# Kernel optimization log

Hardware: AMD Instinct MI355X
Metric: run time of the kernel (lower is better)

## Reference

```python
import jax, jax.numpy as jnp
import numpy as np

B, S, D, H = 2, 2048, 1024, 16
DK = D // H


def setup_inputs() -> dict:
    key = jax.random.key(0)
    ks = jax.random.split(key, 8)
    xavier = lambda k, shape: jax.random.uniform(k, shape, jnp.float32, -1.0, 1.0) * np.sqrt(6.0 / (shape[0] + shape[1]))
    return {
        "query": jax.random.normal(ks[0], (B, S, D), jnp.float32),
        "key": jax.random.normal(ks[1], (B, S, D), jnp.float32),
        "value": jax.random.normal(ks[2], (B, S, D), jnp.float32),
        # causal mask: True above the diagonal -> masked out
        "mask": jnp.broadcast_to(jnp.triu(jnp.ones((S, S), bool), k=1), (B, S, S)),
        "w_q": xavier(ks[3], (D, D)),  # torch Linear weight [out, in]
        "w_k": xavier(ks[4], (D, D)),
        "w_v": xavier(ks[5], (D, D)),
        "w_o": xavier(ks[6], (D, D)),
        "b_o": jnp.zeros((D,), jnp.float32),
    }


def reference(query, key, value, mask, w_q, w_k, w_v, w_o, b_o):
    b, sq, d = query.shape
    sk = key.shape[1]
    # projections (torch Linear: x @ W.T)
    Q = (query @ w_q.T).reshape(b, sq, H, DK).transpose(0, 2, 1, 3)  # [B,H,Sq,DK]
    K = (key @ w_k.T).reshape(b, sk, H, DK).transpose(0, 2, 1, 3)
    V = (value @ w_v.T).reshape(b, sk, H, DK).transpose(0, 2, 1, 3)
    scores = jnp.einsum('bhqd,bhkd->bhqk', Q, K) / np.sqrt(DK)
    scores = jnp.where(mask[:, None, :, :], jnp.float32(-1e9), scores)
    attn = jax.nn.softmax(scores, axis=-1)  # dropout is identity in eval
    out = jnp.einsum('bhqk,bhkd->bhqd', attn, V)
    out = out.transpose(0, 2, 1, 3).reshape(b, sq, d)
    return out @ w_o.T + b_o
```

## Files before the change

kernel.cpp:

```cpp
#include <hip/hip_runtime.h>
#include <hip/hip_bf16.h>
#include <stdint.h>


typedef __attribute__((ext_vector_type(4))) float  f32x4;
typedef __attribute__((ext_vector_type(4))) int    i32x4;
typedef __attribute__((ext_vector_type(8))) __bf16 bf16x8;
typedef __attribute__((ext_vector_type(4))) __bf16 bf16x4;
typedef __attribute__((ext_vector_type(2))) __bf16 bf16x2;

#define MFMA16(a, b, c) __builtin_amdgcn_mfma_f32_16x16x32_bf16((a), (b), (c), 0, 0, 0)

__device__ __forceinline__ void async16(const void* g, void* lds) {
  __builtin_amdgcn_global_load_lds(
      (const __attribute__((address_space(1))) uint32_t*)g,
      (__attribute__((address_space(3))) uint32_t*)lds,
      16, 0, 0);
}

__device__ __forceinline__ bf16x8 lds_swz_read(const __bf16* base, int row, int cchunk) {
  const int sw = cchunk ^ (row & 7);
  return *(const bf16x8*)((const char*)base + row * 128 + sw * 16);
}

__global__ void detect_dtype(const uint16_t* __restrict__ w, int* __restrict__ flag) {
  __shared__ int s;
  if (threadIdx.x == 0) s = 0;
  __syncthreads();
  int big = 0;
  for (int i = threadIdx.x; i < 8192; i += 256) {
    uint32_t u = ((uint32_t)w[i]) << 16;
    float f;
    __builtin_memcpy(&f, &u, 4);
    if (fabsf(f) > 1.0f) big = 1;
  }
  if (big) atomicOr(&s, 1);
  __syncthreads();
  if (threadIdx.x == 0) *flag = s;
}

struct CvtArgs { const void* src[8]; void* dst[8]; int n[8]; };

__global__ __launch_bounds__(256)
void convert_all(CvtArgs a, const int* __restrict__ flagp) {
  if (*flagp == 0) return;
  const int t = blockIdx.y;
  const int n = a.n[t];
  const int i0 = (blockIdx.x * 256 + threadIdx.x) * 8;
  if (i0 >= n) return;
  const float* s = (const float*)a.src[t];
  __bf16* d = (__bf16*)a.dst[t];
  bf16x8 v;
#pragma unroll
  for (int j = 0; j < 8; ++j) v[j] = (__bf16)s[i0 + j];
  *(bf16x8*)(d + i0) = v;
}

struct GemmArgs {
  const __bf16* A[3];    const __bf16* W[3];
  const __bf16* Acvt[3]; const __bf16* Wcvt[3];
  void* C[3]; float scale[3];
  const __bf16* bias; const __bf16* biascvt;
  const int* flagp; int mode;
};

__global__ __launch_bounds__(256, 3)
void gemm_nt(GemmArgs ga)
{
  constexpr int K = 1024;
  __shared__ __align__(16) __bf16 smem[8704];
  __bf16* As = smem;
  __bf16* Bs = smem + 4096;

  const int id = blockIdx.x + (blockIdx.y << 3) + (blockIdx.z << 8);
  const int mb = (id & 7) * 4 + ((id >> 3) & 3);
  const int rest = id >> 5;
  const int nb = rest & 7;
  const int z = rest >> 3;

  const int f = *ga.flagp;
  const __bf16* __restrict__ A = f ? ga.Acvt[z] : ga.A[z];
  const __bf16* __restrict__ W = f ? ga.Wcvt[z] : ga.W[z];
  void* __restrict__ C = ga.C[z];
  const float scale = ga.scale[z];
  const int mode = ga.mode;

  const int tid = threadIdx.x;
  const int lane = tid & 63;
  const int wave = tid >> 6;
  const int l15 = lane & 15;
  const int quad = lane >> 4;
  const int bm = mb * 128;
  const int bn = nb * 128;
  const int wm = (wave >> 1) * 64;
  const int wn = (wave & 1) * 64;

  f32x4 acc[4][4];
#pragma unroll
  for (int mi = 0; mi < 4; ++mi)
#pragma unroll
    for (int ni = 0; ni < 4; ++ni) {
      f32x4 zz = {0.f, 0.f, 0.f, 0.f};
      acc[mi][ni] = zz;
    }

  for (int kt = 0; kt < K / 32; ++kt) {
    const int k0 = kt * 32;
    __syncthreads();
#pragma unroll
    for (int r = 0; r < 2; ++r) {
      const int chunk = r * 256 + wave * 64 + lane;
      const int row = chunk >> 2, c = chunk & 3;
      async16(A + (size_t)(bm + row) * K + k0 + c * 8, As + (r * 256 + wave * 64) * 8);
      async16(W + (size_t)(bn + row) * K + k0 + c * 8, Bs + (r * 256 + wave * 64) * 8);
    }
    __syncthreads();

    bf16x8 af[4];
    bf16x8 bfr[4];
#pragma unroll
    for (int mi = 0; mi < 4; ++mi)
      af[mi] = *(const bf16x8*)(As + (wm + mi * 16 + l15) * 32 + quad * 8);
#pragma unroll
    for (int ni = 0; ni < 4; ++ni)
      bfr[ni] = *(const bf16x8*)(Bs + (wn + ni * 16 + l15) * 32 + quad * 8);
#pragma unroll
    for (int mi = 0; mi < 4; ++mi)
#pragma unroll
      for (int ni = 0; ni < 4; ++ni)
        acc[mi][ni] = MFMA16(af[mi], bfr[ni], acc[mi][ni]);
  }

  float bv[4] = {0.f, 0.f, 0.f, 0.f};
  if (mode == 1) {
    const __bf16* bias = f ? ga.biascvt : ga.bias;
#pragma unroll
    for (int ni = 0; ni < 4; ++ni) bv[ni] = (float)bias[bn + wn + ni * 16 + l15];
  }
  __bf16 (*Cs)[136] = (__bf16(*)[136])smem;

#pragma unroll
  for (int pass = 0; pass < 2; ++pass) {
    __syncthreads();
    if ((wave >> 1) == pass) {
#pragma unroll
      for (int mi = 0; mi < 4; ++mi)
#pragma unroll
        for (int ni = 0; ni < 4; ++ni)
#pragma unroll
          for (int r = 0; r < 4; ++r)
            Cs[mi * 16 + quad * 4 + r][wn + ni * 16 + l15] =
                (__bf16)(acc[mi][ni][r] * scale + bv[ni]);
    }
    __syncthreads();

    if (mode == 0) {
#pragma unroll
      for (int it = 0; it < 4; ++it) {
        const int cid = it * 256 + tid;
        const int off = cid & 7, seg = cid >> 3;
        const int hl = seg & 1, rowl = seg >> 1;
        f32x4 v = *(const f32x4*)(&Cs[rowl][hl * 64 + off * 8]);
        const int m = bm + pass * 64 + rowl;
        const int b = m >> 11, s = m & 2047;
        const int h = (bn >> 6) + hl;
        *(f32x4*)((__bf16*)C + ((size_t)(b * 16 + h) * 2048 + s) * 64 + off * 8) = v;
      }
    } else if (f) {
#pragma unroll
      for (int it = 0; it < 4; ++it) {
        const int cid = it * 256 + tid;
        const int off = cid & 15, rowl = cid >> 4;
        bf16x8 vb = *(const bf16x8*)(&Cs[rowl][off * 8]);
        const int m = bm + pass * 64 + rowl;
        float* dst = (float*)C + (size_t)m * 1024 + bn + off * 8;
        f32x4 lo, hi;
#pragma unroll
        for (int j = 0; j < 4; ++j) { lo[j] = (float)vb[j]; hi[j] = (float)vb[4 + j]; }
        *(f32x4*)dst = lo;
        *(f32x4*)(dst + 4) = hi;
      }
    } else {
#pragma unroll
      for (int it = 0; it < 4; ++it) {
        const int cid = it * 256 + tid;
        const int off = cid & 15, rowl = cid >> 4;
        bf16x8 vb = *(const bf16x8*)(&Cs[rowl][off * 8]);
        const int m = bm + pass * 64 + rowl;
        *(bf16x8*)((__bf16*)C + (size_t)m * 1024 + bn + off * 8) = vb;
      }
    }
  }
}

__global__ __launch_bounds__(256, 3)
void attn(const __bf16* __restrict__ Q,
          const __bf16* __restrict__ Kg,
          const __bf16* __restrict__ Vg,
          __bf16* __restrict__ O)
{
  __shared__ __align__(16) __bf16 Ks[128 * 64];
  __shared__ __align__(16) __bf16 Vts[64][136];
  __shared__ __align__(16) __bf16 PsT[4][16][136];

  const int tid = threadIdx.x;
  const int lane = tid & 63;
  const int wave = tid >> 6;
  const int l15 = lane & 15;
  const int quad = lane >> 4;

  const int zb = blockIdx.x;
  const int qt = 31 - (zb >> 5);
  const int bh = zb & 31;
  const int q0 = qt * 64;
  const int nIter = (qt >> 1) + 1;

  const __bf16* Qp = Q + (size_t)bh * 2048 * 64;
  const __bf16* Kp = Kg + (size_t)bh * 2048 * 64;
  const __bf16* Vp = Vg + (size_t)bh * 2048 * 64;

  const int qrow_wl = wave * 16 + l15;

  bf16x8 qf[2];
#pragma unroll
  for (int kc = 0; kc < 2; ++kc)
    qf[kc] = *(const bf16x8*)(Qp + (size_t)(q0 + qrow_wl) * 64 + kc * 32 + quad * 8);

  f32x4 o_[4];
#pragma unroll
  for (int dt = 0; dt < 4; ++dt) {
    f32x4 zz = {0.f, 0.f, 0.f, 0.f};
    o_[dt] = zz;
  }
  float mrow = -1e30f, lrow = 0.0f;

  for (int ktt = 0; ktt < nIter; ++ktt) {
    const int k0 = ktt * 128;
    __syncthreads();
#pragma unroll
    for (int r = 0; r < 4; ++r) {
      const int chunk = r * 256 + tid;
      const int row = chunk >> 3, c = (chunk & 7) ^ (row & 7);
      async16(Kp + (size_t)(k0 + row) * 64 + c * 8,
              (char*)Ks + (r * 256 + wave * 64) * 16);
    }
#pragma unroll
    for (int rr = 0; rr < 2; ++rr) {
      const int task = rr * 256 + tid;
      const int pp = task & 63, dgg = task >> 6;
      bf16x8 v0 = *(const bf16x8*)(Vp + (size_t)(k0 + 2 * pp) * 64 + dgg * 8);
      bf16x8 v1 = *(const bf16x8*)(Vp + (size_t)(k0 + 2 * pp + 1) * 64 + dgg * 8);
#pragma unroll
      for (int j = 0; j < 8; ++j) {
        bf16x2 pr = { v0[j], v1[j] };
        *(bf16x2*)(&Vts[dgg * 8 + j][2 * pp]) = pr;
      }
    }
    __syncthreads();

    f32x4 st[8];
#pragma unroll
    for (int nt = 0; nt < 8; ++nt) {
      f32x4 zz = {0.f, 0.f, 0.f, 0.f};
      st[nt] = zz;
    }
#pragma unroll
    for (int kc = 0; kc < 2; ++kc)
#pragma unroll
      for (int nt = 0; nt < 8; ++nt) {
        bf16x8 kf = lds_swz_read(Ks, nt * 16 + l15, kc * 4 + quad);
        st[nt] = MFMA16(kf, qf[kc], st[nt]);
      }

    if (ktt == (qt >> 1)) {
#pragma unroll
      for (int nt = 0; nt < 8; ++nt)
#pragma unroll
        for (int r = 0; r < 4; ++r)
          if (k0 + nt * 16 + quad * 4 + r > q0 + qrow_wl) st[nt][r] = -1e30f;
    }

    float tmax = -1e30f;
#pragma unroll
    for (int nt = 0; nt < 8; ++nt)
#pragma unroll
      for (int r = 0; r < 4; ++r) tmax = fmaxf(tmax, st[nt][r]);
    tmax = fmaxf(tmax, __shfl_xor(tmax, 16, 64));
    tmax = fmaxf(tmax, __shfl_xor(tmax, 32, 64));
    const float mnew = fmaxf(mrow, tmax);
    const float alpha = __expf(mrow - mnew);
    float rs = 0.0f;
#pragma unroll
    for (int nt = 0; nt < 8; ++nt) {
      bf16x4 pd;
#pragma unroll
      for (int r = 0; r < 4; ++r) {
        const float pv = __expf(st[nt][r] - mnew);
        rs += pv;
        pd[r] = (__bf16)pv;
      }
      *(bf16x4*)(&PsT[wave][l15][nt * 16 + quad * 4]) = pd;
    }
    rs += __shfl_xor(rs, 16, 64);
    rs += __shfl_xor(rs, 32, 64);
    lrow = lrow * alpha + rs;
    mrow = mnew;
#pragma unroll
    for (int dt = 0; dt < 4; ++dt) o_[dt] *= alpha;

#pragma unroll
    for (int kc = 0; kc < 4; ++kc) {
      bf16x8 pf = *(const bf16x8*)(&PsT[wave][l15][kc * 32 + quad * 8]);
#pragma unroll
      for (int dt = 0; dt < 4; ++dt) {
        bf16x8 vf = *(const bf16x8*)(&Vts[dt * 16 + l15][kc * 32 + quad * 8]);
        o_[dt] = MFMA16(vf, pf, o_[dt]);
      }
    }
  }

  __syncthreads();
  __bf16 (*Ot)[72] = (__bf16(*)[72])&Vts[0][0];
  const float inv_l = 1.0f / lrow;
#pragma unroll
  for (int dt = 0; dt < 4; ++dt)
#pragma unroll
    for (int r = 0; r < 4; r += 2) {
      bf16x2 pr = { (__bf16)(o_[dt][r] * inv_l),
                    (__bf16)(o_[dt][r + 1] * inv_l) };
      *(bf16x2*)(&Ot[qrow_wl][dt * 16 + quad * 4 + r]) = pr;
    }
  __syncthreads();

  const int b = bh >> 4, h = bh & 15;
#pragma unroll
  for (int t = 0; t < 2; ++t) {
    const int i = t * 256 + tid;
    const int row = i >> 3, c = i & 7;
    f32x4 v = *(const f32x4*)(&Ot[row][c * 8]);
    *(f32x4*)(O + (size_t)(b * 2048 + q0 + row) * 1024 + h * 64 + c * 8) = v;
  }
}

extern "C" void kernel_launch(void* const* d_in, const int* in_sizes, int n_in,
                              void* d_out, int out_size, void* d_ws, size_t ws_size,
                              hipStream_t stream) {
  char* ws = (char*)d_ws;
  int* flag = (int*)ws;
  __bf16* Xc0 = (__bf16*)(ws + (1u << 20));
  __bf16* Xc1 = (__bf16*)(ws + (9u << 20));
  __bf16* Xc2 = (__bf16*)(ws + (17u << 20));
  __bf16* Wc0 = (__bf16*)(ws + (25u << 20));
  __bf16* Wc1 = (__bf16*)(ws + (27u << 20));
  __bf16* Wc2 = (__bf16*)(ws + (29u << 20));
  __bf16* Wc3 = (__bf16*)(ws + (31u << 20));
  __bf16* bc  = (__bf16*)(ws + (33u << 20));
  __bf16* Qw  = (__bf16*)(ws + (34u << 20));
  __bf16* Kw  = (__bf16*)(ws + (42u << 20));
  __bf16* Vw  = (__bf16*)(ws + (50u << 20));
  __bf16* Aw  = (__bf16*)(ws + (58u << 20));

  detect_dtype<<<1, 256, 0, stream>>>((const uint16_t*)d_in[4], flag);

  CvtArgs ca;
  ca.src[0] = d_in[0]; ca.dst[0] = Xc0; ca.n[0] = 4194304;
  ca.src[1] = d_in[1]; ca.dst[1] = Xc1; ca.n[1] = 4194304;
  ca.src[2] = d_in[2]; ca.dst[2] = Xc2; ca.n[2] = 4194304;
  ca.src[3] = d_in[4]; ca.dst[3] = Wc0; ca.n[3] = 1048576;
  ca.src[4] = d_in[5]; ca.dst[4] = Wc1; ca.n[4] = 1048576;
  ca.src[5] = d_in[6]; ca.dst[5] = Wc2; ca.n[5] = 1048576;
  ca.src[6] = d_in[7]; ca.dst[6] = Wc3; ca.n[6] = 1048576;
  ca.src[7] = d_in[8]; ca.dst[7] = bc;  ca.n[7] = 1024;
  convert_all<<<dim3(2048, 8), 256, 0, stream>>>(ca, flag);

  GemmArgs g0;
  g0.A[0] = (const __bf16*)d_in[0]; g0.Acvt[0] = Xc0;
  g0.A[1] = (const __bf16*)d_in[1]; g0.Acvt[1] = Xc1;
  g0.A[2] = (const __bf16*)d_in[2]; g0.Acvt[2] = Xc2;
  g0.W[0] = (const __bf16*)d_in[4]; g0.Wcvt[0] = Wc0;
  g0.W[1] = (const __bf16*)d_in[5]; g0.Wcvt[1] = Wc1;
  g0.W[2] = (const __bf16*)d_in[6]; g0.Wcvt[2] = Wc2;
  g0.C[0] = Qw; g0.scale[0] = 0.125f;
  g0.C[1] = Kw; g0.scale[1] = 1.0f;
  g0.C[2] = Vw; g0.scale[2] = 1.0f;
  g0.bias = nullptr; g0.biascvt = nullptr; g0.flagp = flag; g0.mode = 0;
  gemm_nt<<<dim3(8, 32, 3), 256, 0, stream>>>(g0);

  attn<<<dim3(1024), 256, 0, stream>>>(Qw, Kw, Vw, Aw);

  GemmArgs g1;
  g1.A[0] = Aw; g1.Acvt[0] = Aw;
  g1.A[1] = nullptr; g1.Acvt[1] = nullptr;
  g1.A[2] = nullptr; g1.Acvt[2] = nullptr;
  g1.W[0] = (const __bf16*)d_in[7]; g1.Wcvt[0] = Wc3;
  g1.W[1] = nullptr; g1.Wcvt[1] = nullptr;
  g1.W[2] = nullptr; g1.Wcvt[2] = nullptr;
  g1.C[0] = d_out; g1.scale[0] = 1.0f;
  g1.C[1] = nullptr; g1.scale[1] = 0.f;
  g1.C[2] = nullptr; g1.scale[2] = 0.f;
  g1.bias = (const __bf16*)d_in[8]; g1.biascvt = bc;
  g1.flagp = flag; g1.mode = 1;
  gemm_nt<<<dim3(8, 32, 1), 256, 0, stream>>>(g1);
}
```

Measured before the change: 241.2 us.

## Emit V transposed from projection and shrink attention key tile to 64

The V projection epilogue now writes V in a transposed [bh][dk][s] layout. The attention kernel can then load V tiles with async global-to-LDS copies instead of a register-level transpose. The attention key tile drops from 128 to 64, which cuts LDS per block and lets launch bounds target 6 blocks per CU. It also tightens the causal loop bound and reorders the block-to-tile mapping to balance work. Costs are more loop iterations with more syncs, and a strided gather epilogue for V that may cause LDS bank conflicts. The output staging now reuses the P buffer without a barrier, which could race across waves.

Result: no change. 245.4 us (+1.7%).

```diff
diff --git a/kernel.cpp b/kernel.cpp
--- a/kernel.cpp
+++ b/kernel.cpp
@@ -154,7 +154,20 @@
     }
     __syncthreads();
 
-    if (mode == 0) {
+    if (mode == 0 && z == 2) {
+#pragma unroll
+      for (int it = 0; it < 4; ++it) {
+        const int cid = it * 256 + tid;
+        const int n = cid & 127, mg = cid >> 7;
+        bf16x8 vb;
+#pragma unroll
+        for (int i = 0; i < 8; ++i) vb[i] = Cs[mg * 8 + i][n];
+        const int m = bm + pass * 64 + mg * 8;
+        const int b = m >> 11, s = m & 2047;
+        const int h = (bn >> 6) + (n >> 6), dk = n & 63;
+        *(bf16x8*)((__bf16*)C + ((size_t)(b * 16 + h) * 64 + dk) * 2048 + s) = vb;
+      }
+    } else if (mode == 0) {
 #pragma unroll
       for (int it = 0; it < 4; ++it) {
         const int cid = it * 256 + tid;
@@ -193,15 +206,15 @@
   }
 }
 
-__global__ __launch_bounds__(256, 3)
+__global__ __launch_bounds__(256, 6)
 void attn(const __bf16* __restrict__ Q,
           const __bf16* __restrict__ Kg,
-          const __bf16* __restrict__ Vg,
+          const __bf16* __restrict__ Vt,
           __bf16* __restrict__ O)
 {
-  __shared__ __align__(16) __bf16 Ks[128 * 64];
-  __shared__ __align__(16) __bf16 Vts[64][136];
-  __shared__ __align__(16) __bf16 PsT[4][16][136];
+  __shared__ __align__(16) __bf16 Ks[64 * 64];
+  __shared__ __align__(16) __bf16 Vts[64 * 64];
+  __shared__ __align__(16) __bf16 PsT[4][16][72];
 
   const int tid = threadIdx.x;
   const int lane = tid & 63;
@@ -209,15 +222,14 @@
   const int l15 = lane & 15;
   const int quad = lane >> 4;
 
-  const int zb = blockIdx.x;
-  const int qt = 31 - (zb >> 5);
-  const int bh = zb & 31;
+  int zb = blockIdx.x, qt, bh;
+  if (zb < 512) { qt = zb & 31; bh = zb >> 5; }
+  else { int z2 = zb - 512; qt = 31 - (z2 & 31); bh = 16 + (z2 >> 5); }
   const int q0 = qt * 64;
-  const int nIter = (qt >> 1) + 1;
 
   const __bf16* Qp = Q + (size_t)bh * 2048 * 64;
   const __bf16* Kp = Kg + (size_t)bh * 2048 * 64;
-  const __bf16* Vp = Vg + (size_t)bh * 2048 * 64;
+  const __bf16* Vp = Vt + (size_t)bh * 64 * 2048;
 
   const int qrow_wl = wave * 16 + l15;
 
@@ -234,55 +246,45 @@
   }
   float mrow = -1e30f, lrow = 0.0f;
 
-  for (int ktt = 0; ktt < nIter; ++ktt) {
-    const int k0 = ktt * 128;
-    __syncthreads();
-#pragma unroll
-    for (int r = 0; r < 4; ++r) {
+  for (int kt = 0; kt <= qt; ++kt) {
+    const int k0 = kt * 64;
+    __syncthreads();
+#pragma unroll
+    for (int r = 0; r < 2; ++r) {
       const int chunk = r * 256 + tid;
       const int row = chunk >> 3, c = (chunk & 7) ^ (row & 7);
       async16(Kp + (size_t)(k0 + row) * 64 + c * 8,
               (char*)Ks + (r * 256 + wave * 64) * 16);
-    }
-#pragma unroll
-    for (int rr = 0; rr < 2; ++rr) {
-      const int task = rr * 256 + tid;
-      const int pp = task & 63, dgg = task >> 6;
-      bf16x8 v0 = *(const bf16x8*)(Vp + (size_t)(k0 + 2 * pp) * 64 + dgg * 8);
-      bf16x8 v1 = *(const bf16x8*)(Vp + (size_t)(k0 + 2 * pp + 1) * 64 + dgg * 8);
-#pragma unroll
-      for (int j = 0; j < 8; ++j) {
-        bf16x2 pr = { v0[j], v1[j] };
-        *(bf16x2*)(&Vts[dgg * 8 + j][2 * pp]) = pr;
-      }
-    }
-    __syncthreads();
-
-    f32x4 st[8];
-#pragma unroll
-    for (int nt = 0; nt < 8; ++nt) {
+      async16(Vp + (size_t)row * 2048 + k0 + c * 8,
+              (char*)Vts + (r * 256 + wave * 64) * 16);
+    }
+    __syncthreads();
+
+    f32x4 st[4];
+#pragma unroll
+    for (int nt = 0; nt < 4; ++nt) {
       f32x4 zz = {0.f, 0.f, 0.f, 0.f};
       st[nt] = zz;
     }
 #pragma unroll
     for (int kc = 0; kc < 2; ++kc)
 #pragma unroll
-      for (int nt = 0; nt < 8; ++nt) {
+      for (int nt = 0; nt < 4; ++nt) {
         bf16x8 kf = lds_swz_read(Ks, nt * 16 + l15, kc * 4 + quad);
         st[nt] = MFMA16(kf, qf[kc], st[nt]);
       }
 
-    if (ktt == (qt >> 1)) {
-#pragma unroll
-      for (int nt = 0; nt < 8; ++nt)
+    if (kt == qt) {
+#pragma unroll
+      for (int nt = 0; nt < 4; ++nt)
 #pragma unroll
         for (int r = 0; r < 4; ++r)
-          if (k0 + nt * 16 + quad * 4 + r > q0 + qrow_wl) st[nt][r] = -1e30f;
+          if (nt * 16 + quad * 4 + r > qrow_wl) st[nt][r] = -1e30f;
     }
 
     float tmax = -1e30f;
 #pragma unroll
-    for (int nt = 0; nt < 8; ++nt)
+    for (int nt = 0; nt < 4; ++nt)
 #pragma unroll
       for (int r = 0; r < 4; ++r) tmax = fmaxf(tmax, st[nt][r]);
     tmax = fmaxf(tmax, __shfl_xor(tmax, 16, 64));
@@ -291,7 +293,7 @@
     const float alpha = __expf(mrow - mnew);
     float rs = 0.0f;
 #pragma unroll
-    for (int nt = 0; nt < 8; ++nt) {
+    for (int nt = 0; nt < 4; ++nt) {
       bf16x4 pd;
 #pragma unroll
       for (int r = 0; r < 4; ++r) {
@@ -309,18 +311,17 @@
     for (int dt = 0; dt < 4; ++dt) o_[dt] *= alpha;
 
 #pragma unroll
-    for (int kc = 0; kc < 4; ++kc) {
+    for (int kc = 0; kc < 2; ++kc) {
       bf16x8 pf = *(const bf16x8*)(&PsT[wave][l15][kc * 32 + quad * 8]);
 #pragma unroll
       for (int dt = 0; dt < 4; ++dt) {
-        bf16x8 vf = *(const bf16x8*)(&Vts[dt * 16 + l15][kc * 32 + quad * 8]);
+        bf16x8 vf = lds_swz_read(Vts, dt * 16 + l15, kc * 4 + quad);
         o_[dt] = MFMA16(vf, pf, o_[dt]);
       }
     }
   }
 
-  __syncthreads();
-  __bf16 (*Ot)[72] = (__bf16(*)[72])&Vts[0][0];
+  __bf16 (*Ot)[72] = (__bf16(*)[72])&PsT[0][0][0];
   const float inv_l = 1.0f / lrow;
 #pragma unroll
   for (int dt = 0; dt < 4; ++dt)
```
